# Performance work log

Hardware: AMD Instinct MI355X
Metric: run time of the kernel (lower is better)

The kernel has to match this reference:

```python
import jax, jax.numpy as jnp
import numpy as np
import math

V, D, H, DFF, NL, CTX = 32000, 512, 8, 2048, 2, 1024
B, S = 2, 1024

def ln(x, w, eps=1e-5):
    mu = jnp.mean(x, axis=-1, keepdims=True)
    var = jnp.var(x, axis=-1, keepdims=True)
    return (x - mu) / jnp.sqrt(var + eps) * w

def setup_inputs() -> dict:
    key = jax.random.key(0)
    ks = jax.random.split(key, 10)
    inp = {
        "x": jax.random.randint(ks[0], (B, S), 0, V),
        "wte": jax.random.normal(ks[1], (V, D), jnp.float32) * 0.02,
        "wpe": jax.random.normal(ks[2], (CTX + 1, D), jnp.float32) * 0.02,
        "ln_e_w": jnp.ones((D,), jnp.float32),
        "ln_p_w": jnp.ones((D,), jnp.float32),
        "ln_f_w": jnp.ones((D,), jnp.float32),
        "ln_mlp_w": jnp.ones((D,), jnp.float32),
        "W_q_diag": jax.random.normal(ks[3], (H, D), jnp.float32) * 0.02,
        "W_k_diag": jax.random.normal(ks[4], (H, D), jnp.float32) * 0.02,
        "W_o": jax.random.normal(ks[5], (NL, D, D * H), jnp.float32) * (0.02 / math.sqrt(2 * NL)),
        "mlp_w1": jax.random.normal(ks[6], (DFF, D), jnp.float32) * 0.02,
        "mlp_w2": jax.random.normal(ks[7], (D, DFF), jnp.float32) * 0.02,
    }
    return inp

def reference(x, wte, wpe, ln_e_w, ln_p_w, ln_f_w, ln_mlp_w, W_q_diag, W_k_diag, W_o, mlp_w1, mlp_w2):
    Bsz, Sl = x.shape
    e = ln(wte[x], ln_e_w)                       # (B,S,D)
    p = ln(wpe[: Sl + 1], ln_p_w)                # (S+1,D), identical across batch
    Q = p[1:][None, :, :] * W_q_diag[:, None, :]   # (H,S,D)
    K = p[:-1][None, :, :] * W_k_diag[:, None, :]  # (H,S,D)
    krn = jnp.einsum('hsd,htd->hst', Q, K) / math.sqrt(D)
    mask = jnp.tril(jnp.ones((Sl, Sl), bool))
    krn = jnp.where(mask[None], krn, 0.0)        # (H,S,S)
    wn = 1.0 / (jnp.arange(Sl, dtype=jnp.float32) + 1.0)  # W_N diagonal

    f_k = jnp.zeros_like(e)
    for i in range(NL):
        # R = softmax over S of (V,D)@(B,D,S) -> (B,V,S)
        R = jax.nn.softmax(jnp.einsum('vd,bsd->bvs', wte, f_k), axis=-1)
        ex_wte = jnp.einsum('bvs,vd->bsd', R, wte)
        ex_wte = ex_wte / jnp.sum(R, axis=1)[..., None]  # normalize by sum over V
        Vt = e - ex_wte                                   # (B,S,D)
        delta = jnp.einsum('hst,btd->bhsd', krn, Vt)      # (B,H,S,D)
        delta = delta * wn[None, None, :, None]           # W_N row scaling
        delta = jnp.transpose(delta, (0, 2, 1, 3)).reshape(Bsz, Sl, H * D)
        delta = delta @ W_o[i].T                          # (B,S,D)
        f_k = f_k + delta
        # use_ff MLP block
        h = ln(f_k, ln_mlp_w)
        f_k = f_k + jax.nn.gelu(h @ mlp_w1.T, approximate=False) @ mlp_w2.T

    out = ln(f_k, ln_f_w)
    logits = out[:, -1:, :] @ wte.T               # (B,1,V), targets=None branch
    return logits
```

## Files before the change

### kernel.cpp

```cpp
#include <hip/hip_runtime.h>

#define DV   512
#define SV   1024
#define BV   2
#define VV   32000
#define HV   8
#define DFFV 2048
#define NLV  2
#define KCX  25

typedef __bf16 bf16;
typedef __bf16 bf16x4 __attribute__((ext_vector_type(4)));
typedef __bf16 bf16x8 __attribute__((ext_vector_type(8)));
typedef float  f32x4  __attribute__((ext_vector_type(4)));

__device__ __forceinline__ void lds_dma16(const void* g, void* l) {
  __builtin_amdgcn_global_load_lds(
      (const __attribute__((address_space(1))) unsigned int*)g,
      (__attribute__((address_space(3))) unsigned int*)l,
      16, 0, 0);
}

template<typename OUT>
__device__ __forceinline__ void row_ln_512(const float* __restrict__ src,
                                           const float* __restrict__ w,
                                           OUT* __restrict__ dst, int lane) {
  const float4 a = *(const float4*)(src + lane*8);
  const float4 b = *(const float4*)(src + lane*8 + 4);
  float s = a.x+a.y+a.z+a.w + b.x+b.y+b.z+b.w;
  float q = a.x*a.x+a.y*a.y+a.z*a.z+a.w*a.w + b.x*b.x+b.y*b.y+b.z*b.z+b.w*b.w;
#pragma unroll
  for (int off = 32; off > 0; off >>= 1) {
    s += __shfl_down(s, off, 64);
    q += __shfl_down(q, off, 64);
  }
  s = __shfl(s, 0, 64); q = __shfl(q, 0, 64);
  const float mu   = s * (1.0f/512.0f);
  const float rstd = rsqrtf(q * (1.0f/512.0f) - mu*mu + 1e-5f);
  const float4 wa = *(const float4*)(w + lane*8);
  const float4 wb = *(const float4*)(w + lane*8 + 4);
  OUT* d = dst + lane*8;
  d[0] = (OUT)((a.x-mu)*rstd*wa.x);
  d[1] = (OUT)((a.y-mu)*rstd*wa.y);
  d[2] = (OUT)((a.z-mu)*rstd*wa.z);
  d[3] = (OUT)((a.w-mu)*rstd*wa.w);
  d[4] = (OUT)((b.x-mu)*rstd*wb.x);
  d[5] = (OUT)((b.y-mu)*rstd*wb.y);
  d[6] = (OUT)((b.z-mu)*rstd*wb.z);
  d[7] = (OUT)((b.w-mu)*rstd*wb.w);
}

__global__ void embed_wpe_ln_k(const int* __restrict__ x, const float* __restrict__ wte,
                               const float* __restrict__ wpe, const float* __restrict__ we,
                               const float* __restrict__ wp, float* __restrict__ e,
                               float* __restrict__ pn) {
  const int row = blockIdx.x * 4 + (threadIdx.x >> 6);
  const int lane = threadIdx.x & 63;
  if (row < BV*SV) {
    row_ln_512<float>(wte + (long)x[row] * DV, we, e + (long)row * DV, lane);
  } else {
    const int r = row - BV*SV;
    if (r >= SV + 1) return;
    row_ln_512<float>(wpe + (long)r * DV, wp, pn + (long)r * DV, lane);
  }
}

__global__ void final_obuf_k(const float* __restrict__ f_k, const float* __restrict__ fpart,
                             const float* __restrict__ w, float* __restrict__ obuf) {
  const int b = threadIdx.x >> 6;
  if (b >= BV) return;
  const int lane = threadIdx.x & 63;
  const long ro = ((long)b * SV + (SV - 1)) * DV + lane*8;
  float v[8];
  { const float4 a = *(const float4*)(f_k + ro);
    const float4 c = *(const float4*)(f_k + ro + 4);
    v[0]=a.x;v[1]=a.y;v[2]=a.z;v[3]=a.w;v[4]=c.x;v[5]=c.y;v[6]=c.z;v[7]=c.w; }
  for (int c = 0; c < 8; c++) {
    const float* pp = fpart + ((long)(b*8 + c))*SV*DV + (long)(SV-1)*DV + lane*8;
    const float4 a = *(const float4*)pp;
    const float4 d = *(const float4*)(pp + 4);
    v[0]+=a.x;v[1]+=a.y;v[2]+=a.z;v[3]+=a.w;v[4]+=d.x;v[5]+=d.y;v[6]+=d.z;v[7]+=d.w;
  }
  float s = 0.f, q = 0.f;
#pragma unroll
  for (int k = 0; k < 8; k++) { s += v[k]; q += v[k]*v[k]; }
#pragma unroll
  for (int off = 32; off > 0; off >>= 1) {
    s += __shfl_down(s, off, 64);
    q += __shfl_down(q, off, 64);
  }
  s = __shfl(s, 0, 64); q = __shfl(q, 0, 64);
  const float mu   = s * (1.0f/512.0f);
  const float rstd = rsqrtf(q * (1.0f/512.0f) - mu*mu + 1e-5f);
  const float4 wa = *(const float4*)(w + lane*8);
  const float4 wb = *(const float4*)(w + lane*8 + 4);
  float* d = obuf + (long)b * DV + lane*8;
  d[0] = (v[0]-mu)*rstd*wa.x;
  d[1] = (v[1]-mu)*rstd*wa.y;
  d[2] = (v[2]-mu)*rstd*wa.z;
  d[3] = (v[3]-mu)*rstd*wa.w;
  d[4] = (v[4]-mu)*rstd*wb.x;
  d[5] = (v[5]-mu)*rstd*wb.y;
  d[6] = (v[6]-mu)*rstd*wb.z;
  d[7] = (v[7]-mu)*rstd*wb.w;
}

__global__ void cast3_f2b_k(const float* __restrict__ Wo, const float* __restrict__ w1,
                            const float* __restrict__ w2, bf16* __restrict__ Wob,
                            bf16* __restrict__ w1b, bf16* __restrict__ w2b) {
  const long n0 = (long)NLV*DV*HV*DV, n1 = (long)DFFV*DV, n2 = (long)DV*DFFV;
  long i = ((long)blockIdx.x * 256 + threadIdx.x) * 4;
  const float* in; bf16* o; long r;
  if (i < n0)            { in = Wo; o = Wob; r = i; }
  else if (i < n0 + n1)  { in = w1; o = w1b; r = i - n0; }
  else if (i < n0+n1+n2) { in = w2; o = w2b; r = i - n0 - n1; }
  else return;
  const float4 v = *(const float4*)(in + r);
  bf16x4 ob; ob[0]=(bf16)v.x; ob[1]=(bf16)v.y; ob[2]=(bf16)v.z; ob[3]=(bf16)v.w;
  *(bf16x4*)(&o[r]) = ob;
}

__global__ void wte_prep_k(const float* __restrict__ wte, bf16* __restrict__ wb,
                           bf16* __restrict__ wbT, float* __restrict__ wm) {
  __shared__ float t[32][33];
  __shared__ float cpart[8][32];
  const int d0 = blockIdx.x * 32, v0 = blockIdx.y * 32;
  const int tx = threadIdx.x, ty = threadIdx.y;
  float csum = 0.f;
#pragma unroll
  for (int k = 0; k < 4; k++) {
    const int vl = ty*4 + k;
    const float val = wte[(long)(v0+vl)*DV + d0+tx];
    t[vl][tx] = val;
    csum += val;
  }
  cpart[ty][tx] = csum;
  __syncthreads();
  const int tid = ty*32 + tx;
  const int r = tid >> 3, c = (tid & 7) * 4;
  {
    bf16x4 o;
    o[0] = (bf16)t[r][c];   o[1] = (bf16)t[r][c+1];
    o[2] = (bf16)t[r][c+2]; o[3] = (bf16)t[r][c+3];
    *(bf16x4*)(&wb[(long)(v0+r)*DV + d0+c]) = o;
  }
  {
    bf16x4 o;
    o[0] = (bf16)t[c][r];   o[1] = (bf16)t[c+1][r];
    o[2] = (bf16)t[c+2][r]; o[3] = (bf16)t[c+3][r];
    *(bf16x4*)(&wbT[(long)(d0+r)*VV + v0+c]) = o;
  }
  if (ty == 0) {
    float s = 0.f;
#pragma unroll
    for (int k = 0; k < 8; k++) s += cpart[k][tx];
    atomicAdd(&wm[d0+tx], s);
  }
}

__global__ void qk_prep_k(const float* __restrict__ pn, const float* __restrict__ Wq,
                          const float* __restrict__ Wk, bf16* __restrict__ Qh,
                          bf16* __restrict__ Kh) {
  const int s = blockIdx.x, hh = blockIdx.y;
  const int d = threadIdx.x * 4;
  const float4 q  = *(const float4*)(pn + (long)(s+1)*DV + d);
  const float4 kk = *(const float4*)(pn + (long)s*DV + d);
  const float4 aq = *(const float4*)(Wq + (long)hh*DV + d);
  const float4 ak = *(const float4*)(Wk + (long)hh*DV + d);
  const long o = ((long)hh*SV + s)*DV + d;
  Qh[o+0]=(bf16)(q.x*aq.x);  Qh[o+1]=(bf16)(q.y*aq.y);
  Qh[o+2]=(bf16)(q.z*aq.z);  Qh[o+3]=(bf16)(q.w*aq.w);
  Kh[o+0]=(bf16)(kk.x*ak.x); Kh[o+1]=(bf16)(kk.y*ak.y);
  Kh[o+2]=(bf16)(kk.z*ak.z); Kh[o+3]=(bf16)(kk.w*ak.w);
}

__global__ void freduce_ln_k(const float* __restrict__ part, float* __restrict__ f_k,
                             const float* __restrict__ w, bf16* __restrict__ hbuf,
                             int KC, int init) {
  const int row = blockIdx.x * 4 + (threadIdx.x >> 6);
  const int lane = threadIdx.x & 63;
  const int b = row >> 10;
  const long ro = (long)row * DV + lane*8;
  const long po = (long)(row & (SV-1)) * DV + lane*8;
  float v[8];
  if (init) {
#pragma unroll
    for (int k = 0; k < 8; k++) v[k] = 0.f;
  } else {
    const float4 a = *(const float4*)(f_k + ro);
    const float4 c = *(const float4*)(f_k + ro + 4);
    v[0]=a.x;v[1]=a.y;v[2]=a.z;v[3]=a.w;v[4]=c.x;v[5]=c.y;v[6]=c.z;v[7]=c.w;
  }
  for (int c = 0; c < KC; c++) {
    const float* pp = part + ((long)(b*KC + c))*SV*DV + po;
    const float4 a = *(const float4*)pp;
    const float4 d = *(const float4*)(pp + 4);
    v[0]+=a.x;v[1]+=a.y;v[2]+=a.z;v[3]+=a.w;v[4]+=d.x;v[5]+=d.y;v[6]+=d.z;v[7]+=d.w;
  }
  { float4 o1={v[0],v[1],v[2],v[3]}, o2={v[4],v[5],v[6],v[7]};
    *(float4*)(f_k + ro) = o1; *(float4*)(f_k + ro + 4) = o2; }
  float s = 0.f, q = 0.f;
#pragma unroll
  for (int k = 0; k < 8; k++) { s += v[k]; q += v[k]*v[k]; }
#pragma unroll
  for (int off = 32; off > 0; off >>= 1) {
    s += __shfl_down(s, off, 64);
    q += __shfl_down(q, off, 64);
  }
  s = __shfl(s, 0, 64); q = __shfl(q, 0, 64);
  const float mu   = s * (1.0f/512.0f);
  const float rstd = rsqrtf(q * (1.0f/512.0f) - mu*mu + 1e-5f);
  const float4 wa = *(const float4*)(w + lane*8);
  const float4 wb = *(const float4*)(w + lane*8 + 4);
  bf16* d = hbuf + (long)row * DV + lane*8;
  d[0] = (bf16)((v[0]-mu)*rstd*wa.x);
  d[1] = (bf16)((v[1]-mu)*rstd*wa.y);
  d[2] = (bf16)((v[2]-mu)*rstd*wa.z);
  d[3] = (bf16)((v[3]-mu)*rstd*wa.w);
  d[4] = (bf16)((v[4]-mu)*rstd*wb.x);
  d[5] = (bf16)((v[5]-mu)*rstd*wb.y);
  d[6] = (bf16)((v[6]-mu)*rstd*wb.z);
  d[7] = (bf16)((v[7]-mu)*rstd*wb.w);
}

__global__ void freduce_cast_k(const float* __restrict__ part, float* __restrict__ f_k,
                               bf16* __restrict__ fb, int KC, int do_cast) {
  const long i = ((long)blockIdx.x * 256 + threadIdx.x) * 4;
  const int  b = (int)(i / ((long)SV*DV));
  const long r = i % ((long)SV*DV);
  float4 acc = *(const float4*)(f_k + i);
  for (int c = 0; c < KC; c++) {
    const float4 v = *(const float4*)(part + ((long)(b*KC + c))*SV*DV + r);
    acc.x += v.x; acc.y += v.y; acc.z += v.z; acc.w += v.w;
  }
  *(float4*)(f_k + i) = acc;
  if (do_cast) {
    bf16x4 o; o[0]=(bf16)acc.x; o[1]=(bf16)acc.y; o[2]=(bf16)acc.z; o[3]=(bf16)acc.w;
    *(bf16x4*)(&fb[i]) = o;
  }
}

__global__ void vt_part_k(const float* __restrict__ e, const bf16* __restrict__ pb,
                          const float* __restrict__ part, bf16* __restrict__ VtT) {
  __shared__ float t[32][33];
  __shared__ float cpart[8][32];
  __shared__ float csum[32];
  const int d0 = blockIdx.x * 32, s0 = blockIdx.y * 32;
  const int tx = threadIdx.x, ty = threadIdx.y;
  {
    float cs = 0.f;
    for (int v = ty; v < VV/128; v += 8) cs += part[(long)v * SV + s0 + tx];
    cpart[ty][tx] = cs;
  }
  __syncthreads();
  if (ty == 0) {
    float s = 0.f;
#pragma unroll
    for (int k = 0; k < 8; k++) s += cpart[k][tx];
    csum[tx] = s;
  }
  __syncthreads();
#pragma unroll
  for (int k = 0; k < 4; k++) {
    const int sl = ty + k*8;
    const long off = (long)(s0+sl)*DV + d0+tx;
    float acc = 0.f;
    for (int c = 0; c < KCX; c++) acc += (float)pb[(long)c*SV*DV + off];
    t[sl][tx] = e[off] - acc / csum[sl];
  }
  __syncthreads();
#pragma unroll
  for (int k = 0; k < 4; k++) {
    const int dl = ty + k*8;
    VtT[(long)(d0+dl)*SV + s0+tx] = (bf16)t[tx][dl];
  }
}

__global__ void vt0_transpose_k(const float* __restrict__ e, const float* __restrict__ wm,
                                bf16* __restrict__ VtT) {
  __shared__ float t[32][33];
  const int d0 = blockIdx.x * 32, s0 = blockIdx.y * 32, b = blockIdx.z;
  const int tx = threadIdx.x, ty = threadIdx.y;
  const float* eb = e + (long)b*SV*DV;
  bf16* vb = VtT + (long)b*DV*SV;
  const float mval = wm[d0 + tx] * (1.0f / (float)VV);
#pragma unroll
  for (int k = 0; k < 4; k++) {
    const int sl = ty + k*8;
    t[sl][tx] = eb[(long)(s0+sl)*DV + d0+tx] - mval;
  }
  __syncthreads();
#pragma unroll
  for (int k = 0; k < 4; k++) {
    const int dl = ty + k*8;
    vb[(long)(d0+dl)*SV + s0+tx] = (bf16)t[tx][dl];
  }
}

__global__ void logits_k(const float* __restrict__ obuf, const float* __restrict__ wte,
                         float* __restrict__ out, int V) {
  const int wv = threadIdx.x >> 6, lane = threadIdx.x & 63;
  const int v = blockIdx.x * 4 + wv;
  const float* wr = wte + (long)v * DV;
  const float4 a  = *(const float4*)(wr + lane*8);
  const float4 c  = *(const float4*)(wr + lane*8 + 4);
  const float4 oa0 = *(const float4*)(obuf + lane*8);
  const float4 ob0 = *(const float4*)(obuf + lane*8 + 4);
  const float4 oa1 = *(const float4*)(obuf + DV + lane*8);
  const float4 ob1 = *(const float4*)(obuf + DV + lane*8 + 4);
  float d0 = a.x*oa0.x + a.y*oa0.y + a.z*oa0.z + a.w*oa0.w
           + c.x*ob0.x + c.y*ob0.y + c.z*ob0.z + c.w*ob0.w;
  float d1 = a.x*oa1.x + a.y*oa1.y + a.z*oa1.z + a.w*oa1.w
           + c.x*ob1.x + c.y*ob1.y + c.z*ob1.z + c.w*ob1.w;
#pragma unroll
  for (int off = 32; off > 0; off >>= 1) {
    d0 += __shfl_down(d0, off, 64);
    d1 += __shfl_down(d1, off, 64);
  }
  if (lane == 0) { out[v] = d0; out[(long)V + v] = d1; }
}

__device__ __forceinline__ long xcd_swz(long lin, long nwg) {
  const long qq = nwg >> 3, rr = nwg & 7;
  const long xcd = lin & 7, idx = lin >> 3;
  return (xcd < rr ? xcd * (qq + 1) : rr * (qq + 1) + (xcd - rr) * qq) + idx;
}

struct GemmArgs {
  const bf16* A; const bf16* B;
  float* Cf; bf16* Cb;
  int K, lda, ldb, ldc;
  long sAh, sAb, sBh, sBb, sCh, sCb;
  int Hmod, KC, causal, swap;
  float scale;
};

template<int EPI>
__global__ __launch_bounds__(256)
void gemm_nt(GemmArgs g) {
  __shared__ bf16 As[2][128*32];
  __shared__ bf16 Bs[2][128*32];
  const int tid = threadIdx.x;
  int bx = blockIdx.x, by = blockIdx.y, z = blockIdx.z;
  {
    const int nbx = gridDim.x, nby = gridDim.y;
    const long nwg = (long)nbx * nby * gridDim.z;
    long lin = xcd_swz(bx + (long)nbx * (by + (long)nby * z), nwg);
    bx = (int)(lin % nbx);
    const long t2 = lin / nbx;
    by = (int)(t2 % nby);
    z  = (int)(t2 / nby);
  }
  const int chunk = z % g.KC;
  const int zo = z / g.KC;
  const int h = zo % g.Hmod;
  const int b = zo / g.Hmod;
  if (g.swap) { int t = bx; bx = by; by = t; }
  const int m0 = by * 128;
  const int n0 = bx * 128;
  const long coff = (long)h * g.sCh + (long)b * g.sCb;

  if (EPI == 3 && n0 > m0 + 127) return;

  const bf16* A = g.A + (long)h * g.sAh + (long)b * g.sAb;
  const bf16* B = g.B + (long)h * g.sBh + (long)b * g.sBb;
  const int lane = tid & 63;
  const int wv = tid >> 6;
  const int wm = (wv >> 1) * 64;
  const int wn = (wv & 1) * 64;
  const int frow = lane & 15;
  const int quad = lane >> 4;
  const int sg8  = ((lane & 3) ^ ((lane >> 3) & 3)) * 8;
  const int drow = lane >> 2;

  const f32x4 fzero = {0.f, 0.f, 0.f, 0.f};
  f32x4 acc[4][4];
#pragma unroll
  for (int i = 0; i < 4; i++)
#pragma unroll
    for (int j = 0; j < 4; j++) acc[i][j] = fzero;

  int k0, klen;
  if (g.causal) { k0 = 0; klen = min(g.K, m0 + 128); }
  else          { klen = g.K / g.KC; k0 = chunk * klen; }

  auto stage = [&](int buf, int kk) {
#pragma unroll
    for (int c = 0; c < 2; c++) {
      const int rb = c*64 + wv*16;
      lds_dma16(A + (long)(m0 + rb + drow) * g.lda + kk + sg8, &As[buf][rb*32]);
      lds_dma16(B + (long)(n0 + rb + drow) * g.ldb + kk + sg8, &Bs[buf][rb*32]);
    }
  };

  const int nsteps = klen >> 5;
  int cur = 0;
  stage(0, k0);
  for (int it = 0; it < nsteps; ++it) {
    if (it + 1 < nsteps) {
      stage(cur ^ 1, k0 + (it + 1) * 32);
      asm volatile("s_waitcnt vmcnt(4)" ::: "memory");
    } else {
      asm volatile("s_waitcnt vmcnt(0)" ::: "memory");
    }
    __builtin_amdgcn_s_barrier();
    bf16x8 af[4], bfr[4];
    const int sw = (frow >> 1) & 3;
#pragma unroll
    for (int i = 0; i < 4; i++)
      af[i] = *(const bf16x8*)(&As[cur][(wm + i*16 + frow)*32 + ((quad ^ sw))*8]);
#pragma unroll
    for (int j = 0; j < 4; j++)
      bfr[j] = *(const bf16x8*)(&Bs[cur][(wn + j*16 + frow)*32 + ((quad ^ sw))*8]);
#pragma unroll
    for (int i = 0; i < 4; i++)
#pragma unroll
      for (int j = 0; j < 4; j++)
        acc[i][j] = __builtin_amdgcn_mfma_f32_16x16x32_bf16(af[i], bfr[j], acc[i][j], 0, 0, 0);
    __builtin_amdgcn_s_barrier();
    cur ^= 1;
  }

  const int rb = quad * 4;
#pragma unroll
  for (int i = 0; i < 4; i++) {
#pragma unroll
    for (int j = 0; j < 4; j++) {
#pragma unroll
      for (int r = 0; r < 4; r++) {
        const int gm = m0 + wm + i*16 + rb + r;
        const int gn = n0 + wn + j*16 + frow;
        const float v = acc[i][j][r];
        if (EPI == 2) {
          g.Cb[coff + (long)gm * g.ldc + gn] = (bf16)v;
        } else if (EPI == 3) {
          const float val = (gn <= gm) ? v * g.scale / (float)(gm + 1) : 0.0f;
          g.Cb[coff + (long)gm * g.ldc + gn] = (bf16)val;
        } else if (EPI == 4) {
          const float ge = 0.5f * v * (1.0f + erff(v * 0.70710678118f));
          g.Cb[coff + (long)gm * g.ldc + gn] = (bf16)ge;
        } else if (EPI == 6) {
          g.Cf[(long)(b*g.KC + chunk) * g.sCh + (long)gm * g.ldc + gn] = v;
        }
      }
    }
  }
}

template<int EPI>
__global__ __launch_bounds__(512)
void gemm256(GemmArgs g) {
  __shared__ bf16 As[2][256*64];
  __shared__ bf16 Bs[2][256*64];
  const int tid = threadIdx.x;
  int bm = blockIdx.x, bn = blockIdx.y, z = blockIdx.z;
  {
    const int nbx = gridDim.x, nby = gridDim.y;
    const long nwg = (long)nbx * nby * gridDim.z;
    long lin = xcd_swz(bm + (long)nbx * (bn + (long)nby * z), nwg);
    bm = (int)(lin % nbx);
    const long t2 = lin / nbx;
    bn = (int)(t2 % nby);
    z  = (int)(t2 / nby);
  }
  const int m0 = bm * 256, n0 = bn * 256;
  const int lane = tid & 63, wv = tid >> 6;
  const int wm = (wv >> 2) * 128, wn = (wv & 3) * 64;
  const int frow = lane & 15, quad = lane >> 4;
  const int sg8  = ((lane & 7) ^ (lane >> 3)) * 8;
  const int drow = lane >> 3;

  const f32x4 fzero = {0.f, 0.f, 0.f, 0.f};
  f32x4 acc[8][4];
#pragma unroll
  for (int i = 0; i < 8; i++)
#pragma unroll
    for (int j = 0; j < 4; j++) acc[i][j] = fzero;

  const int klen = g.K / g.KC;
  const int k0 = z * klen;

  auto stage = [&](int buf, int kk) {
#pragma unroll
    for (int c = 0; c < 4; c++) {
      const int rb = c*64 + wv*8;
      lds_dma16(g.A + (long)(m0 + rb + drow) * g.lda + kk + sg8, &As[buf][rb*64]);
      lds_dma16(g.B + (long)(n0 + rb + drow) * g.ldb + kk + sg8, &Bs[buf][rb*64]);
    }
  };

  const int nsteps = klen >> 6;
  int cur = 0;
  stage(0, k0);
  for (int it = 0; it < nsteps; ++it) {
    if (it + 1 < nsteps) {
      stage(cur ^ 1, k0 + (it + 1) * 64);
      asm volatile("s_waitcnt vmcnt(8)" ::: "memory");
    } else {
      asm volatile("s_waitcnt vmcnt(0)" ::: "memory");
    }
    __builtin_amdgcn_s_barrier();
    const int sw = frow & 7;
#pragma unroll
    for (int ks = 0; ks < 2; ks++) {
      bf16x8 af[8], bfr[4];
#pragma unroll
      for (int j = 0; j < 4; j++)
        bfr[j] = *(const bf16x8*)(&Bs[cur][(wn + j*16 + frow)*64 + (((ks*4 + quad) ^ sw))*8]);
#pragma unroll
      for (int i = 0; i < 8; i++)
        af[i] = *(const bf16x8*)(&As[cur][(wm + i*16 + frow)*64 + (((ks*4 + quad) ^ sw))*8]);
#pragma unroll
      for (int i = 0; i < 8; i++)
#pragma unroll
        for (int j = 0; j < 4; j++)
          acc[i][j] = __builtin_amdgcn_mfma_f32_16x16x32_bf16(af[i], bfr[j], acc[i][j], 0, 0, 0);
    }
    __builtin_amdgcn_s_barrier();
    cur ^= 1;
  }

  const int rb4 = quad * 4;
  if (EPI == 5) {
    const int vblk = (n0 + wn) >> 7;
#pragma unroll
    for (int i = 0; i < 8; i++) {
#pragma unroll
      for (int r = 0; r < 4; r++) {
        const int gm = m0 + wm + i*16 + rb4 + r;
        float rs = 0.f;
#pragma unroll
        for (int j = 0; j < 4; j++) {
          const int gn = n0 + wn + j*16 + frow;
          const float ev = __expf(acc[i][j][r]);
          g.Cb[(long)gm * g.ldc + gn] = (bf16)ev;
          rs += ev;
        }
#pragma unroll
        for (int off = 1; off < 16; off <<= 1)
          rs += __shfl_xor(rs, off, 64);
        if (frow == 0) atomicAdd(g.Cf + (long)vblk * SV + gm, rs);
      }
    }
  } else {
#pragma unroll
    for (int i = 0; i < 8; i++) {
#pragma unroll
      for (int j = 0; j < 4; j++) {
#pragma unroll
        for (int r = 0; r < 4; r++) {
          const int gm = m0 + wm + i*16 + rb4 + r;
          const int gn = n0 + wn + j*16 + frow;
          g.Cb[(long)z * g.sCh + (long)gm * g.ldc + gn] = (bf16)acc[i][j][r];
        }
      }
    }
  }
}

static void layer_tail(int il, bf16* krn, bf16* VtT, bf16* U_rs, bf16* Wo_b,
                       float* f_k, bf16* f_k_b, bf16* hbuf, bf16* Gbuf, float* fpart,
                       bf16* w1_b, bf16* w2_b, const float* lnmw, int do_cast,
                       int init, int last, hipStream_t stream) {
  {
    GemmArgs g = {};
    g.A = krn; g.B = VtT; g.Cb = U_rs;
    g.K = SV; g.lda = SV; g.ldb = SV; g.ldc = HV*DV;
    g.sAh = (long)SV*SV; g.sBb = (long)DV*SV;
    g.sCh = DV; g.sCb = (long)SV*HV*DV;
    g.Hmod = HV; g.KC = 1; g.causal = 1;
    gemm_nt<2><<<dim3(DV/128, SV/128, BV*HV), 256, 0, stream>>>(g);
  }
  {
    GemmArgs g = {};
    g.A = U_rs; g.B = Wo_b + (long)il*DV*HV*DV; g.Cf = fpart;
    g.K = HV*DV; g.lda = HV*DV; g.ldb = HV*DV; g.ldc = DV;
    g.sAb = (long)SV*HV*DV; g.sCh = (long)SV*DV;
    g.Hmod = 1; g.KC = 8; g.causal = 0;
    gemm_nt<6><<<dim3(DV/128, SV/128, BV*8), 256, 0, stream>>>(g);
  }
  freduce_ln_k<<<dim3(BV*SV/4), 256, 0, stream>>>(fpart, f_k, lnmw, hbuf, 8, init);
  {
    GemmArgs g = {};
    g.A = hbuf; g.B = w1_b; g.Cb = Gbuf;
    g.K = DV; g.lda = DV; g.ldb = DV; g.ldc = DFFV;
    g.sAb = (long)SV*DV; g.sCb = (long)SV*DFFV;
    g.Hmod = 1; g.KC = 1; g.causal = 0;
    gemm_nt<4><<<dim3(DFFV/128, SV/128, BV), 256, 0, stream>>>(g);
  }
  {
    GemmArgs g = {};
    g.A = Gbuf; g.B = w2_b; g.Cf = fpart;
    g.K = DFFV; g.lda = DFFV; g.ldb = DFFV; g.ldc = DV;
    g.sAb = (long)SV*DFFV; g.sCh = (long)SV*DV;
    g.Hmod = 1; g.KC = 8; g.causal = 0;
    gemm_nt<6><<<dim3(DV/128, SV/128, BV*8), 256, 0, stream>>>(g);
  }
  if (!last)
    freduce_cast_k<<<dim3(BV*SV*DV/4/256), 256, 0, stream>>>(fpart, f_k, f_k_b, 8, do_cast);
}

extern "C" void kernel_launch(void* const* d_in, const int* in_sizes, int n_in,
                              void* d_out, int out_size, void* d_ws, size_t ws_size,
                              hipStream_t stream) {
  const int*   x    = (const int*)d_in[0];
  const float* wte  = (const float*)d_in[1];
  const float* wpe  = (const float*)d_in[2];
  const float* lnew = (const float*)d_in[3];
  const float* lnpw = (const float*)d_in[4];
  const float* lnfw = (const float*)d_in[5];
  const float* lnmw = (const float*)d_in[6];
  const float* Wq   = (const float*)d_in[7];
  const float* Wk   = (const float*)d_in[8];
  const float* Wo   = (const float*)d_in[9];
  const float* w1   = (const float*)d_in[10];
  const float* w2   = (const float*)d_in[11];
  float* out = (float*)d_out;
  (void)in_sizes; (void)n_in; (void)out_size; (void)ws_size;

  char* p = (char*)d_ws;
  auto alloc = [&](size_t bytes) -> void* {
    void* r = (void*)p;
    p += (bytes + 255) & ~(size_t)255;
    return r;
  };
  float* e      = (float*)alloc((size_t)BV*SV*DV*4);
  float* pn     = (float*)alloc((size_t)(SV+1)*DV*4);
  bf16*  wteT_b = (bf16*)alloc((size_t)DV*VV*2);
  bf16*  wte_b  = (bf16*)alloc((size_t)VV*DV*2);
  bf16*  krn    = (bf16*)alloc((size_t)HV*SV*SV*2);
  bf16*  Wo_b   = (bf16*)alloc((size_t)NLV*DV*HV*DV*2);
  bf16*  w1_b   = (bf16*)alloc((size_t)DFFV*DV*2);
  bf16*  w2_b   = (bf16*)alloc((size_t)DV*DFFV*2);
  float* f_k    = (float*)alloc((size_t)BV*SV*DV*4);
  bf16*  f_k_b  = (bf16*)alloc((size_t)BV*SV*DV*2);
  bf16*  expart = (bf16*)alloc((size_t)KCX*SV*DV*2);
  bf16*  VtT    = (bf16*)alloc((size_t)BV*DV*SV*2);
  bf16*  hbuf   = (bf16*)alloc((size_t)BV*SV*DV*2);
  float* part   = (float*)alloc((size_t)BV*(VV/128)*SV*4);
  float* obuf   = (float*)alloc((size_t)BV*DV*4);
  float* wmean  = (float*)alloc((size_t)DV*4);
  char*  arena  = (char*)alloc((size_t)SV*VV*2);
  bf16*  Qh     = (bf16*)arena;
  bf16*  Kh     = (bf16*)(arena + (size_t)HV*SV*DV*2);
  bf16*  PT     = (bf16*)arena;
  bf16*  U_rs   = (bf16*)arena;
  bf16*  Gbuf   = (bf16*)(arena + (size_t)BV*SV*HV*DV*2);
  float* fpart  = (float*)(arena + (size_t)BV*SV*HV*DV*2 + (size_t)BV*SV*DFFV*2);

  hipMemsetAsync(wmean, 0, (size_t)DV*4, stream);
  hipMemsetAsync(part, 0, (size_t)BV*(VV/128)*SV*4, stream);
  wte_prep_k<<<dim3(DV/32, VV/32), dim3(32,8), 0, stream>>>(wte, wte_b, wteT_b, wmean);
  cast3_f2b_k<<<dim3((NLV*DV*HV*DV + DFFV*DV + DV*DFFV)/4/256), 256, 0, stream>>>(
      Wo, w1, w2, Wo_b, w1_b, w2_b);
  embed_wpe_ln_k<<<dim3((BV*SV + SV+1 + 3)/4), 256, 0, stream>>>(
      x, wte, wpe, lnew, lnpw, e, pn);
  qk_prep_k<<<dim3(SV, HV), 128, 0, stream>>>(pn, Wq, Wk, Qh, Kh);

  {
    GemmArgs g = {};
    g.A = Qh; g.B = Kh; g.Cb = krn;
    g.K = DV; g.lda = DV; g.ldb = DV; g.ldc = SV;
    g.sAh = (long)SV*DV; g.sBh = (long)SV*DV; g.sCh = (long)SV*SV;
    g.Hmod = HV; g.KC = 1; g.causal = 0;
    g.scale = 0.044194173824159216f;
    gemm_nt<3><<<dim3(SV/128, SV/128, HV), 256, 0, stream>>>(g);
  }

  vt0_transpose_k<<<dim3(DV/32, SV/32, BV), dim3(32,8), 0, stream>>>(e, wmean, VtT);
  layer_tail(0, krn, VtT, U_rs, Wo_b, f_k, f_k_b, hbuf, Gbuf, fpart,
             w1_b, w2_b, lnmw, 1, 1, 0, stream);

  for (int b = 0; b < BV; b++) {
    float* partb = part + (long)b*(VV/128)*SV;
    {
      GemmArgs g = {};
      g.A = f_k_b + (long)b*SV*DV; g.B = wte_b; g.Cb = PT; g.Cf = partb;
      g.K = DV; g.lda = DV; g.ldb = DV; g.ldc = VV;
      g.KC = 1;
      gemm256<5><<<dim3(SV/256, VV/256, 1), 512, 0, stream>>>(g);
    }
    {
      GemmArgs g = {};
      g.A = PT; g.B = wteT_b; g.Cb = expart;
      g.K = VV; g.lda = VV; g.ldb = VV; g.ldc = DV;
      g.sCh = (long)SV*DV;
      g.KC = KCX;
      gemm256<7><<<dim3(SV/256, DV/256, KCX), 512, 0, stream>>>(g);
    }
    vt_part_k<<<dim3(DV/32, SV/32), dim3(32,8), 0, stream>>>(
        e + (long)b*SV*DV, expart, partb, VtT + (long)b*DV*SV);
  }
  layer_tail(1, krn, VtT, U_rs, Wo_b, f_k, f_k_b, hbuf, Gbuf, fpart,
             w1_b, w2_b, lnmw, 0, 0, 1, stream);

  final_obuf_k<<<1, 128, 0, stream>>>(f_k, fpart, lnfw, obuf);
  logits_k<<<dim3(VV/4), 256, 0, stream>>>(obuf, wte, out, VV);
}
```

Before: 500.1 us.

## Compute only the last sequence position in the final layer via GEMVs

The output needs only the logits of the last token, so the final layer's attention-delta, output projection and MLP are now computed just for row S-1. This is done with a dot-product kernel plus a chain of GEMV kernels instead of the full-sequence GEMMs and reductions. The first layer is specialised into its own tail function, and several helper kernels are moved earlier in the file. This removes most of the second layer's matrix work, in exchange for several small, latency-bound launches.

```diff
diff --git a/kernel.cpp b/kernel.cpp
--- a/kernel.cpp
+++ b/kernel.cpp
@@ -65,22 +65,304 @@
   }
 }
 
-__global__ void final_obuf_k(const float* __restrict__ f_k, const float* __restrict__ fpart,
-                             const float* __restrict__ w, float* __restrict__ obuf) {
+__global__ void cast3_f2b_k(const float* __restrict__ Wo, const float* __restrict__ w1,
+                            const float* __restrict__ w2, bf16* __restrict__ Wob,
+                            bf16* __restrict__ w1b, bf16* __restrict__ w2b) {
+  const long n0 = (long)NLV*DV*HV*DV, n1 = (long)DFFV*DV, n2 = (long)DV*DFFV;
+  long i = ((long)blockIdx.x * 256 + threadIdx.x) * 4;
+  const float* in; bf16* o; long r;
+  if (i < n0)            { in = Wo; o = Wob; r = i; }
+  else if (i < n0 + n1)  { in = w1; o = w1b; r = i - n0; }
+  else if (i < n0+n1+n2) { in = w2; o = w2b; r = i - n0 - n1; }
+  else return;
+  const float4 v = *(const float4*)(in + r);
+  bf16x4 ob; ob[0]=(bf16)v.x; ob[1]=(bf16)v.y; ob[2]=(bf16)v.z; ob[3]=(bf16)v.w;
+  *(bf16x4*)(&o[r]) = ob;
+}
+
+__global__ void wte_prep_k(const float* __restrict__ wte, bf16* __restrict__ wb,
+                           bf16* __restrict__ wbT, float* __restrict__ wm) {
+  __shared__ float t[32][33];
+  __shared__ float cpart[8][32];
+  const int d0 = blockIdx.x * 32, v0 = blockIdx.y * 32;
+  const int tx = threadIdx.x, ty = threadIdx.y;
+  float csum = 0.f;
+#pragma unroll
+  for (int k = 0; k < 4; k++) {
+    const int vl = ty*4 + k;
+    const float val = wte[(long)(v0+vl)*DV + d0+tx];
+    t[vl][tx] = val;
+    csum += val;
+  }
+  cpart[ty][tx] = csum;
+  __syncthreads();
+  const int tid = ty*32 + tx;
+  const int r = tid >> 3, c = (tid & 7) * 4;
+  {
+    bf16x4 o;
+    o[0] = (bf16)t[r][c];   o[1] = (bf16)t[r][c+1];
+    o[2] = (bf16)t[r][c+2]; o[3] = (bf16)t[r][c+3];
+    *(bf16x4*)(&wb[(long)(v0+r)*DV + d0+c]) = o;
+  }
+  {
+    bf16x4 o;
+    o[0] = (bf16)t[c][r];   o[1] = (bf16)t[c+1][r];
+    o[2] = (bf16)t[c+2][r]; o[3] = (bf16)t[c+3][r];
+    *(bf16x4*)(&wbT[(long)(d0+r)*VV + v0+c]) = o;
+  }
+  if (ty == 0) {
+    float s = 0.f;
+#pragma unroll
+    for (int k = 0; k < 8; k++) s += cpart[k][tx];
+    atomicAdd(&wm[d0+tx], s);
+  }
+}
+
+__global__ void qk_prep_k(const float* __restrict__ pn, const float* __restrict__ Wq,
+                          const float* __restrict__ Wk, bf16* __restrict__ Qh,
+                          bf16* __restrict__ Kh) {
+  const int s = blockIdx.x, hh = blockIdx.y;
+  const int d = threadIdx.x * 4;
+  const float4 q  = *(const float4*)(pn + (long)(s+1)*DV + d);
+  const float4 kk = *(const float4*)(pn + (long)s*DV + d);
+  const float4 aq = *(const float4*)(Wq + (long)hh*DV + d);
+  const float4 ak = *(const float4*)(Wk + (long)hh*DV + d);
+  const long o = ((long)hh*SV + s)*DV + d;
+  Qh[o+0]=(bf16)(q.x*aq.x);  Qh[o+1]=(bf16)(q.y*aq.y);
+  Qh[o+2]=(bf16)(q.z*aq.z);  Qh[o+3]=(bf16)(q.w*aq.w);
+  Kh[o+0]=(bf16)(kk.x*ak.x); Kh[o+1]=(bf16)(kk.y*ak.y);
+  Kh[o+2]=(bf16)(kk.z*ak.z); Kh[o+3]=(bf16)(kk.w*ak.w);
+}
+
+__global__ void freduce_ln_k(const float* __restrict__ part, float* __restrict__ f_k,
+                             const float* __restrict__ w, bf16* __restrict__ hbuf,
+                             int KC, int init) {
+  const int row = blockIdx.x * 4 + (threadIdx.x >> 6);
+  const int lane = threadIdx.x & 63;
+  const int b = row >> 10;
+  const long ro = (long)row * DV + lane*8;
+  const long po = (long)(row & (SV-1)) * DV + lane*8;
+  float v[8];
+  if (init) {
+#pragma unroll
+    for (int k = 0; k < 8; k++) v[k] = 0.f;
+  } else {
+    const float4 a = *(const float4*)(f_k + ro);
+    const float4 c = *(const float4*)(f_k + ro + 4);
+    v[0]=a.x;v[1]=a.y;v[2]=a.z;v[3]=a.w;v[4]=c.x;v[5]=c.y;v[6]=c.z;v[7]=c.w;
+  }
+  for (int c = 0; c < KC; c++) {
+    const float* pp = part + ((long)(b*KC + c))*SV*DV + po;
+    const float4 a = *(const float4*)pp;
+    const float4 d = *(const float4*)(pp + 4);
+    v[0]+=a.x;v[1]+=a.y;v[2]+=a.z;v[3]+=a.w;v[4]+=d.x;v[5]+=d.y;v[6]+=d.z;v[7]+=d.w;
+  }
+  { float4 o1={v[0],v[1],v[2],v[3]}, o2={v[4],v[5],v[6],v[7]};
+    *(float4*)(f_k + ro) = o1; *(float4*)(f_k + ro + 4) = o2; }
+  float s = 0.f, q = 0.f;
+#pragma unroll
+  for (int k = 0; k < 8; k++) { s += v[k]; q += v[k]*v[k]; }
+#pragma unroll
+  for (int off = 32; off > 0; off >>= 1) {
+    s += __shfl_down(s, off, 64);
+    q += __shfl_down(q, off, 64);
+  }
+  s = __shfl(s, 0, 64); q = __shfl(q, 0, 64);
+  const float mu   = s * (1.0f/512.0f);
+  const float rstd = rsqrtf(q * (1.0f/512.0f) - mu*mu + 1e-5f);
+  const float4 wa = *(const float4*)(w + lane*8);
+  const float4 wb = *(const float4*)(w + lane*8 + 4);
+  bf16* d = hbuf + (long)row * DV + lane*8;
+  d[0] = (bf16)((v[0]-mu)*rstd*wa.x);
+  d[1] = (bf16)((v[1]-mu)*rstd*wa.y);
+  d[2] = (bf16)((v[2]-mu)*rstd*wa.z);
+  d[3] = (bf16)((v[3]-mu)*rstd*wa.w);
+  d[4] = (bf16)((v[4]-mu)*rstd*wb.x);
+  d[5] = (bf16)((v[5]-mu)*rstd*wb.y);
+  d[6] = (bf16)((v[6]-mu)*rstd*wb.z);
+  d[7] = (bf16)((v[7]-mu)*rstd*wb.w);
+}
+
+__global__ void freduce_cast_k(const float* __restrict__ part, float* __restrict__ f_k,
+                               bf16* __restrict__ fb, int KC, int do_cast) {
+  const long i = ((long)blockIdx.x * 256 + threadIdx.x) * 4;
+  const int  b = (int)(i / ((long)SV*DV));
+  const long r = i % ((long)SV*DV);
+  float4 acc = *(const float4*)(f_k + i);
+  for (int c = 0; c < KC; c++) {
+    const float4 v = *(const float4*)(part + ((long)(b*KC + c))*SV*DV + r);
+    acc.x += v.x; acc.y += v.y; acc.z += v.z; acc.w += v.w;
+  }
+  *(float4*)(f_k + i) = acc;
+  if (do_cast) {
+    bf16x4 o; o[0]=(bf16)acc.x; o[1]=(bf16)acc.y; o[2]=(bf16)acc.z; o[3]=(bf16)acc.w;
+    *(bf16x4*)(&fb[i]) = o;
+  }
+}
+
+__global__ void vt_part_k(const float* __restrict__ e, const bf16* __restrict__ pb,
+                          const float* __restrict__ part, bf16* __restrict__ VtT) {
+  __shared__ float t[32][33];
+  __shared__ float cpart[8][32];
+  __shared__ float csum[32];
+  const int d0 = blockIdx.x * 32, s0 = blockIdx.y * 32;
+  const int tx = threadIdx.x, ty = threadIdx.y;
+  {
+    float cs = 0.f;
+    for (int v = ty; v < VV/128; v += 8) cs += part[(long)v * SV + s0 + tx];
+    cpart[ty][tx] = cs;
+  }
+  __syncthreads();
+  if (ty == 0) {
+    float s = 0.f;
+#pragma unroll
+    for (int k = 0; k < 8; k++) s += cpart[k][tx];
+    csum[tx] = s;
+  }
+  __syncthreads();
+#pragma unroll
+  for (int k = 0; k < 4; k++) {
+    const int sl = ty + k*8;
+    const long off = (long)(s0+sl)*DV + d0+tx;
+    float acc = 0.f;
+    for (int c = 0; c < KCX; c++) acc += (float)pb[(long)c*SV*DV + off];
+    t[sl][tx] = e[off] - acc / csum[sl];
+  }
+  __syncthreads();
+#pragma unroll
+  for (int k = 0; k < 4; k++) {
+    const int dl = ty + k*8;
+    VtT[(long)(d0+dl)*SV + s0+tx] = (bf16)t[tx][dl];
+  }
+}
+
+__global__ void vt0_transpose_k(const float* __restrict__ e, const float* __restrict__ wm,
+                                bf16* __restrict__ VtT) {
+  __shared__ float t[32][33];
+  const int d0 = blockIdx.x * 32, s0 = blockIdx.y * 32, b = blockIdx.z;
+  const int tx = threadIdx.x, ty = threadIdx.y;
+  const float* eb = e + (long)b*SV*DV;
+  bf16* vb = VtT + (long)b*DV*SV;
+  const float mval = wm[d0 + tx] * (1.0f / (float)VV);
+#pragma unroll
+  for (int k = 0; k < 4; k++) {
+    const int sl = ty + k*8;
+    t[sl][tx] = eb[(long)(s0+sl)*DV + d0+tx] - mval;
+  }
+  __syncthreads();
+#pragma unroll
+  for (int k = 0; k < 4; k++) {
+    const int dl = ty + k*8;
+    vb[(long)(d0+dl)*SV + s0+tx] = (bf16)t[tx][dl];
+  }
+}
+
+
+__global__ void u_last_k(const bf16* __restrict__ krn, const bf16* __restrict__ VtT,
+                         bf16* __restrict__ u) {
+  const int wv = threadIdx.x >> 6, lane = threadIdx.x & 63;
+  const int d = blockIdx.x * 4 + wv;
+  const int h = blockIdx.y, b = blockIdx.z;
+  const bf16* kr = krn + (long)h*SV*SV + (long)(SV-1)*SV;
+  const bf16* vr = VtT + (long)b*DV*SV + (long)d*SV;
+  float acc = 0.f;
+#pragma unroll
+  for (int it = 0; it < 2; it++) {
+    const int k = lane*8 + it*512;
+    const bf16x8 a = *(const bf16x8*)(kr + k);
+    const bf16x8 v = *(const bf16x8*)(vr + k);
+#pragma unroll
+    for (int i = 0; i < 8; i++) acc += (float)a[i] * (float)v[i];
+  }
+#pragma unroll
+  for (int off = 32; off > 0; off >>= 1) acc += __shfl_down(acc, off, 64);
+  if (lane == 0) u[((long)b*HV + h)*DV + d] = (bf16)acc;
+}
+
+template<int ACT>
+__global__ void gemv_k(const bf16* __restrict__ W, const bf16* __restrict__ vec,
+                       float* __restrict__ outf, bf16* __restrict__ outb,
+                       int M, int K, long sVb) {
+  const int wv = threadIdx.x >> 6, lane = threadIdx.x & 63;
+  const int m = blockIdx.x * 4 + wv;
+  const int b = blockIdx.y;
+  if (m >= M) return;
+  const bf16* wr = W + (long)m * K;
+  const bf16* vb = vec + (long)b * sVb;
+  float acc = 0.f;
+  for (int k = lane*8; k < K; k += 512) {
+    const bf16x8 a = *(const bf16x8*)(wr + k);
+    const bf16x8 v = *(const bf16x8*)(vb + k);
+#pragma unroll
+    for (int i = 0; i < 8; i++) acc += (float)a[i] * (float)v[i];
+  }
+#pragma unroll
+  for (int off = 32; off > 0; off >>= 1) acc += __shfl_down(acc, off, 64);
+  if (lane == 0) {
+    if (ACT == 0) outf[(long)b * M + m] = acc;
+    else {
+      const float ge = 0.5f * acc * (1.0f + erff(acc * 0.70710678118f));
+      outb[(long)b * M + m] = (bf16)ge;
+    }
+  }
+}
+
+__global__ void mid_ln_k(const float* __restrict__ f_k, const float* __restrict__ delta,
+                         const float* __restrict__ w, float* __restrict__ f_last,
+                         bf16* __restrict__ h) {
   const int b = threadIdx.x >> 6;
   if (b >= BV) return;
   const int lane = threadIdx.x & 63;
   const long ro = ((long)b * SV + (SV - 1)) * DV + lane*8;
+  const float* dp = delta + (long)b * DV + lane*8;
   float v[8];
   { const float4 a = *(const float4*)(f_k + ro);
     const float4 c = *(const float4*)(f_k + ro + 4);
-    v[0]=a.x;v[1]=a.y;v[2]=a.z;v[3]=a.w;v[4]=c.x;v[5]=c.y;v[6]=c.z;v[7]=c.w; }
-  for (int c = 0; c < 8; c++) {
-    const float* pp = fpart + ((long)(b*8 + c))*SV*DV + (long)(SV-1)*DV + lane*8;
-    const float4 a = *(const float4*)pp;
-    const float4 d = *(const float4*)(pp + 4);
-    v[0]+=a.x;v[1]+=a.y;v[2]+=a.z;v[3]+=a.w;v[4]+=d.x;v[5]+=d.y;v[6]+=d.z;v[7]+=d.w;
-  }
+    const float4 da = *(const float4*)dp;
+    const float4 db = *(const float4*)(dp + 4);
+    v[0]=a.x+da.x; v[1]=a.y+da.y; v[2]=a.z+da.z; v[3]=a.w+da.w;
+    v[4]=c.x+db.x; v[5]=c.y+db.y; v[6]=c.z+db.z; v[7]=c.w+db.w; }
+  { float* fl = f_last + (long)b*DV + lane*8;
+    float4 o1={v[0],v[1],v[2],v[3]}, o2v={v[4],v[5],v[6],v[7]};
+    *(float4*)fl = o1; *(float4*)(fl+4) = o2v; }
+  float s = 0.f, q = 0.f;
+#pragma unroll
+  for (int k = 0; k < 8; k++) { s += v[k]; q += v[k]*v[k]; }
+#pragma unroll
+  for (int off = 32; off > 0; off >>= 1) {
+    s += __shfl_down(s, off, 64);
+    q += __shfl_down(q, off, 64);
+  }
+  s = __shfl(s, 0, 64); q = __shfl(q, 0, 64);
+  const float mu   = s * (1.0f/512.0f);
+  const float rstd = rsqrtf(q * (1.0f/512.0f) - mu*mu + 1e-5f);
+  const float4 wa = *(const float4*)(w + lane*8);
+  const float4 wb = *(const float4*)(w + lane*8 + 4);
+  bf16* d = h + (long)b * DV + lane*8;
+  d[0] = (bf16)((v[0]-mu)*rstd*wa.x);
+  d[1] = (bf16)((v[1]-mu)*rstd*wa.y);
+  d[2] = (bf16)((v[2]-mu)*rstd*wa.z);
+  d[3] = (bf16)((v[3]-mu)*rstd*wa.w);
+  d[4] = (bf16)((v[4]-mu)*rstd*wb.x);
+  d[5] = (bf16)((v[5]-mu)*rstd*wb.y);
+  d[6] = (bf16)((v[6]-mu)*rstd*wb.z);
+  d[7] = (bf16)((v[7]-mu)*rstd*wb.w);
+}
+
+__global__ void final2_k(const float* __restrict__ f_last, const float* __restrict__ o2,
+                         const float* __restrict__ w, float* __restrict__ obuf) {
+  const int b = threadIdx.x >> 6;
+  if (b >= BV) return;
+  const int lane = threadIdx.x & 63;
+  const float* fl = f_last + (long)b * DV + lane*8;
+  const float* op = o2 + (long)b * DV + lane*8;
+  float v[8];
+  { const float4 a = *(const float4*)fl;
+    const float4 c = *(const float4*)(fl + 4);
+    const float4 da = *(const float4*)op;
+    const float4 db = *(const float4*)(op + 4);
+    v[0]=a.x+da.x; v[1]=a.y+da.y; v[2]=a.z+da.z; v[3]=a.w+da.w;
+    v[4]=c.x+db.x; v[5]=c.y+db.y; v[6]=c.z+db.z; v[7]=c.w+db.w; }
   float s = 0.f, q = 0.f;
 #pragma unroll
   for (int k = 0; k < 8; k++) { s += v[k]; q += v[k]*v[k]; }
@@ -103,198 +385,6 @@
   d[5] = (v[5]-mu)*rstd*wb.y;
   d[6] = (v[6]-mu)*rstd*wb.z;
   d[7] = (v[7]-mu)*rstd*wb.w;
-}
-
-__global__ void cast3_f2b_k(const float* __restrict__ Wo, const float* __restrict__ w1,
-                            const float* __restrict__ w2, bf16* __restrict__ Wob,
-                            bf16* __restrict__ w1b, bf16* __restrict__ w2b) {
-  const long n0 = (long)NLV*DV*HV*DV, n1 = (long)DFFV*DV, n2 = (long)DV*DFFV;
-  long i = ((long)blockIdx.x * 256 + threadIdx.x) * 4;
-  const float* in; bf16* o; long r;
-  if (i < n0)            { in = Wo; o = Wob; r = i; }
-  else if (i < n0 + n1)  { in = w1; o = w1b; r = i - n0; }
-  else if (i < n0+n1+n2) { in = w2; o = w2b; r = i - n0 - n1; }
-  else return;
-  const float4 v = *(const float4*)(in + r);
-  bf16x4 ob; ob[0]=(bf16)v.x; ob[1]=(bf16)v.y; ob[2]=(bf16)v.z; ob[3]=(bf16)v.w;
-  *(bf16x4*)(&o[r]) = ob;
-}
-
-__global__ void wte_prep_k(const float* __restrict__ wte, bf16* __restrict__ wb,
-                           bf16* __restrict__ wbT, float* __restrict__ wm) {
-  __shared__ float t[32][33];
-  __shared__ float cpart[8][32];
-  const int d0 = blockIdx.x * 32, v0 = blockIdx.y * 32;
-  const int tx = threadIdx.x, ty = threadIdx.y;
-  float csum = 0.f;
-#pragma unroll
-  for (int k = 0; k < 4; k++) {
-    const int vl = ty*4 + k;
-    const float val = wte[(long)(v0+vl)*DV + d0+tx];
-    t[vl][tx] = val;
-    csum += val;
-  }
-  cpart[ty][tx] = csum;
-  __syncthreads();
-  const int tid = ty*32 + tx;
-  const int r = tid >> 3, c = (tid & 7) * 4;
-  {
-    bf16x4 o;
-    o[0] = (bf16)t[r][c];   o[1] = (bf16)t[r][c+1];
-    o[2] = (bf16)t[r][c+2]; o[3] = (bf16)t[r][c+3];
-    *(bf16x4*)(&wb[(long)(v0+r)*DV + d0+c]) = o;
-  }
-  {
-    bf16x4 o;
-    o[0] = (bf16)t[c][r];   o[1] = (bf16)t[c+1][r];
-    o[2] = (bf16)t[c+2][r]; o[3] = (bf16)t[c+3][r];
-    *(bf16x4*)(&wbT[(long)(d0+r)*VV + v0+c]) = o;
-  }
-  if (ty == 0) {
-    float s = 0.f;
-#pragma unroll
-    for (int k = 0; k < 8; k++) s += cpart[k][tx];
-    atomicAdd(&wm[d0+tx], s);
-  }
-}
-
-__global__ void qk_prep_k(const float* __restrict__ pn, const float* __restrict__ Wq,
-                          const float* __restrict__ Wk, bf16* __restrict__ Qh,
-                          bf16* __restrict__ Kh) {
-  const int s = blockIdx.x, hh = blockIdx.y;
-  const int d = threadIdx.x * 4;
-  const float4 q  = *(const float4*)(pn + (long)(s+1)*DV + d);
-  const float4 kk = *(const float4*)(pn + (long)s*DV + d);
-  const float4 aq = *(const float4*)(Wq + (long)hh*DV + d);
-  const float4 ak = *(const float4*)(Wk + (long)hh*DV + d);
-  const long o = ((long)hh*SV + s)*DV + d;
-  Qh[o+0]=(bf16)(q.x*aq.x);  Qh[o+1]=(bf16)(q.y*aq.y);
-  Qh[o+2]=(bf16)(q.z*aq.z);  Qh[o+3]=(bf16)(q.w*aq.w);
-  Kh[o+0]=(bf16)(kk.x*ak.x); Kh[o+1]=(bf16)(kk.y*ak.y);
-  Kh[o+2]=(bf16)(kk.z*ak.z); Kh[o+3]=(bf16)(kk.w*ak.w);
-}
-
-__global__ void freduce_ln_k(const float* __restrict__ part, float* __restrict__ f_k,
-                             const float* __restrict__ w, bf16* __restrict__ hbuf,
-                             int KC, int init) {
-  const int row = blockIdx.x * 4 + (threadIdx.x >> 6);
-  const int lane = threadIdx.x & 63;
-  const int b = row >> 10;
-  const long ro = (long)row * DV + lane*8;
-  const long po = (long)(row & (SV-1)) * DV + lane*8;
-  float v[8];
-  if (init) {
-#pragma unroll
-    for (int k = 0; k < 8; k++) v[k] = 0.f;
-  } else {
-    const float4 a = *(const float4*)(f_k + ro);
-    const float4 c = *(const float4*)(f_k + ro + 4);
-    v[0]=a.x;v[1]=a.y;v[2]=a.z;v[3]=a.w;v[4]=c.x;v[5]=c.y;v[6]=c.z;v[7]=c.w;
-  }
-  for (int c = 0; c < KC; c++) {
-    const float* pp = part + ((long)(b*KC + c))*SV*DV + po;
-    const float4 a = *(const float4*)pp;
-    const float4 d = *(const float4*)(pp + 4);
-    v[0]+=a.x;v[1]+=a.y;v[2]+=a.z;v[3]+=a.w;v[4]+=d.x;v[5]+=d.y;v[6]+=d.z;v[7]+=d.w;
-  }
-  { float4 o1={v[0],v[1],v[2],v[3]}, o2={v[4],v[5],v[6],v[7]};
-    *(float4*)(f_k + ro) = o1; *(float4*)(f_k + ro + 4) = o2; }
-  float s = 0.f, q = 0.f;
-#pragma unroll
-  for (int k = 0; k < 8; k++) { s += v[k]; q += v[k]*v[k]; }
-#pragma unroll
-  for (int off = 32; off > 0; off >>= 1) {
-    s += __shfl_down(s, off, 64);
-    q += __shfl_down(q, off, 64);
-  }
-  s = __shfl(s, 0, 64); q = __shfl(q, 0, 64);
-  const float mu   = s * (1.0f/512.0f);
-  const float rstd = rsqrtf(q * (1.0f/512.0f) - mu*mu + 1e-5f);
-  const float4 wa = *(const float4*)(w + lane*8);
-  const float4 wb = *(const float4*)(w + lane*8 + 4);
-  bf16* d = hbuf + (long)row * DV + lane*8;
-  d[0] = (bf16)((v[0]-mu)*rstd*wa.x);
-  d[1] = (bf16)((v[1]-mu)*rstd*wa.y);
-  d[2] = (bf16)((v[2]-mu)*rstd*wa.z);
-  d[3] = (bf16)((v[3]-mu)*rstd*wa.w);
-  d[4] = (bf16)((v[4]-mu)*rstd*wb.x);
-  d[5] = (bf16)((v[5]-mu)*rstd*wb.y);
-  d[6] = (bf16)((v[6]-mu)*rstd*wb.z);
-  d[7] = (bf16)((v[7]-mu)*rstd*wb.w);
-}
-
-__global__ void freduce_cast_k(const float* __restrict__ part, float* __restrict__ f_k,
-                               bf16* __restrict__ fb, int KC, int do_cast) {
-  const long i = ((long)blockIdx.x * 256 + threadIdx.x) * 4;
-  const int  b = (int)(i / ((long)SV*DV));
-  const long r = i % ((long)SV*DV);
-  float4 acc = *(const float4*)(f_k + i);
-  for (int c = 0; c < KC; c++) {
-    const float4 v = *(const float4*)(part + ((long)(b*KC + c))*SV*DV + r);
-    acc.x += v.x; acc.y += v.y; acc.z += v.z; acc.w += v.w;
-  }
-  *(float4*)(f_k + i) = acc;
-  if (do_cast) {
-    bf16x4 o; o[0]=(bf16)acc.x; o[1]=(bf16)acc.y; o[2]=(bf16)acc.z; o[3]=(bf16)acc.w;
-    *(bf16x4*)(&fb[i]) = o;
-  }
-}
-
-__global__ void vt_part_k(const float* __restrict__ e, const bf16* __restrict__ pb,
-                          const float* __restrict__ part, bf16* __restrict__ VtT) {
-  __shared__ float t[32][33];
-  __shared__ float cpart[8][32];
-  __shared__ float csum[32];
-  const int d0 = blockIdx.x * 32, s0 = blockIdx.y * 32;
-  const int tx = threadIdx.x, ty = threadIdx.y;
-  {
-    float cs = 0.f;
-    for (int v = ty; v < VV/128; v += 8) cs += part[(long)v * SV + s0 + tx];
-    cpart[ty][tx] = cs;
-  }
-  __syncthreads();
-  if (ty == 0) {
-    float s = 0.f;
-#pragma unroll
-    for (int k = 0; k < 8; k++) s += cpart[k][tx];
-    csum[tx] = s;
-  }
-  __syncthreads();
-#pragma unroll
-  for (int k = 0; k < 4; k++) {
-    const int sl = ty + k*8;
-    const long off = (long)(s0+sl)*DV + d0+tx;
-    float acc = 0.f;
-    for (int c = 0; c < KCX; c++) acc += (float)pb[(long)c*SV*DV + off];
-    t[sl][tx] = e[off] - acc / csum[sl];
-  }
-  __syncthreads();
-#pragma unroll
-  for (int k = 0; k < 4; k++) {
-    const int dl = ty + k*8;
-    VtT[(long)(d0+dl)*SV + s0+tx] = (bf16)t[tx][dl];
-  }
-}
-
-__global__ void vt0_transpose_k(const float* __restrict__ e, const float* __restrict__ wm,
-                                bf16* __restrict__ VtT) {
-  __shared__ float t[32][33];
-  const int d0 = blockIdx.x * 32, s0 = blockIdx.y * 32, b = blockIdx.z;
-  const int tx = threadIdx.x, ty = threadIdx.y;
-  const float* eb = e + (long)b*SV*DV;
-  bf16* vb = VtT + (long)b*DV*SV;
-  const float mval = wm[d0 + tx] * (1.0f / (float)VV);
-#pragma unroll
-  for (int k = 0; k < 4; k++) {
-    const int sl = ty + k*8;
-    t[sl][tx] = eb[(long)(s0+sl)*DV + d0+tx] - mval;
-  }
-  __syncthreads();
-#pragma unroll
-  for (int k = 0; k < 4; k++) {
-    const int dl = ty + k*8;
-    vb[(long)(d0+dl)*SV + s0+tx] = (bf16)t[tx][dl];
-  }
 }
 
 __global__ void logits_k(const float* __restrict__ obuf, const float* __restrict__ wte,
@@ -558,10 +648,9 @@
   }
 }
 
-static void layer_tail(int il, bf16* krn, bf16* VtT, bf16* U_rs, bf16* Wo_b,
-                       float* f_k, bf16* f_k_b, bf16* hbuf, bf16* Gbuf, float* fpart,
-                       bf16* w1_b, bf16* w2_b, const float* lnmw, int do_cast,
-                       int init, int last, hipStream_t stream) {
+static void layer_tail0(bf16* krn, bf16* VtT, bf16* U_rs, bf16* Wo_b,
+                        float* f_k, bf16* f_k_b, bf16* hbuf, bf16* Gbuf, float* fpart,
+                        bf16* w1_b, bf16* w2_b, const float* lnmw, hipStream_t stream) {
   {
     GemmArgs g = {};
     g.A = krn; g.B = VtT; g.Cb = U_rs;
@@ -573,13 +662,13 @@
   }
   {
     GemmArgs g = {};
-    g.A = U_rs; g.B = Wo_b + (long)il*DV*HV*DV; g.Cf = fpart;
+    g.A = U_rs; g.B = Wo_b; g.Cf = fpart;
     g.K = HV*DV; g.lda = HV*DV; g.ldb = HV*DV; g.ldc = DV;
     g.sAb = (long)SV*HV*DV; g.sCh = (long)SV*DV;
     g.Hmod = 1; g.KC = 8; g.causal = 0;
     gemm_nt<6><<<dim3(DV/128, SV/128, BV*8), 256, 0, stream>>>(g);
   }
-  freduce_ln_k<<<dim3(BV*SV/4), 256, 0, stream>>>(fpart, f_k, lnmw, hbuf, 8, init);
+  freduce_ln_k<<<dim3(BV*SV/4), 256, 0, stream>>>(fpart, f_k, lnmw, hbuf, 8, 1);
   {
     GemmArgs g = {};
     g.A = hbuf; g.B = w1_b; g.Cb = Gbuf;
@@ -596,8 +685,7 @@
     g.Hmod = 1; g.KC = 8; g.causal = 0;
     gemm_nt<6><<<dim3(DV/128, SV/128, BV*8), 256, 0, stream>>>(g);
   }
-  if (!last)
-    freduce_cast_k<<<dim3(BV*SV*DV/4/256), 256, 0, stream>>>(fpart, f_k, f_k_b, 8, do_cast);
+  freduce_cast_k<<<dim3(BV*SV*DV/4/256), 256, 0, stream>>>(fpart, f_k, f_k_b, 8, 1);
 }
 
 extern "C" void kernel_launch(void* const* d_in, const int* in_sizes, int n_in,
@@ -640,6 +728,12 @@
   float* part   = (float*)alloc((size_t)BV*(VV/128)*SV*4);
   float* obuf   = (float*)alloc((size_t)BV*DV*4);
   float* wmean  = (float*)alloc((size_t)DV*4);
+  bf16*  u_last = (bf16*)alloc((size_t)BV*HV*DV*2);
+  float* delta  = (float*)alloc((size_t)BV*DV*4);
+  float* f_last = (float*)alloc((size_t)BV*DV*4);
+  bf16*  h_last = (bf16*)alloc((size_t)BV*DV*2);
+  bf16*  g_last = (bf16*)alloc((size_t)BV*DFFV*2);
+  float* o2buf  = (float*)alloc((size_t)BV*DV*4);
   char*  arena  = (char*)alloc((size_t)SV*VV*2);
   bf16*  Qh     = (bf16*)arena;
   bf16*  Kh     = (bf16*)(arena + (size_t)HV*SV*DV*2);
@@ -668,8 +762,8 @@
   }
 
   vt0_transpose_k<<<dim3(DV/32, SV/32, BV), dim3(32,8), 0, stream>>>(e, wmean, VtT);
-  layer_tail(0, krn, VtT, U_rs, Wo_b, f_k, f_k_b, hbuf, Gbuf, fpart,
-             w1_b, w2_b, lnmw, 1, 1, 0, stream);
+  layer_tail0(krn, VtT, U_rs, Wo_b, f_k, f_k_b, hbuf, Gbuf, fpart,
+              w1_b, w2_b, lnmw, stream);
 
   for (int b = 0; b < BV; b++) {
     float* partb = part + (long)b*(VV/128)*SV;
@@ -691,9 +785,15 @@
     vt_part_k<<<dim3(DV/32, SV/32), dim3(32,8), 0, stream>>>(
         e + (long)b*SV*DV, expart, partb, VtT + (long)b*DV*SV);
   }
-  layer_tail(1, krn, VtT, U_rs, Wo_b, f_k, f_k_b, hbuf, Gbuf, fpart,
-             w1_b, w2_b, lnmw, 0, 0, 1, stream);
-
-  final_obuf_k<<<1, 128, 0, stream>>>(f_k, fpart, lnfw, obuf);
+
+  u_last_k<<<dim3(DV/4, HV, BV), 256, 0, stream>>>(krn, VtT, u_last);
+  gemv_k<0><<<dim3(DV/4, BV), 256, 0, stream>>>(
+      Wo_b + (long)1*DV*HV*DV, u_last, delta, nullptr, DV, HV*DV, (long)HV*DV);
+  mid_ln_k<<<1, 128, 0, stream>>>(f_k, delta, lnmw, f_last, h_last);
+  gemv_k<1><<<dim3(DFFV/4, BV), 256, 0, stream>>>(
+      w1_b, h_last, nullptr, g_last, DFFV, DV, (long)DV);
+  gemv_k<0><<<dim3(DV/4, BV), 256, 0, stream>>>(
+      w2_b, g_last, o2buf, nullptr, DV, DFFV, (long)DFFV);
+  final2_k<<<1, 128, 0, stream>>>(f_last, o2buf, lnfw, obuf);
   logits_k<<<dim3(VV/4), 256, 0, stream>>>(obuf, wte, out, VV);
 }
```

Result: faster. 438.1 us (-12.4%).
